# Kernel tuning notes

Hardware: AMD Instinct MI355X
Metric: run time of the kernel (lower is better)

The kernel has to match this reference:

```python
import jax, jax.numpy as jnp
import numpy as np

B, S, HID, NH = 8, 1024, 1024, 16
DH = HID // NH
ZERO = 1e-8  # undefined repo constant, assumed small epsilon


def setup_inputs() -> dict:
    key = jax.random.key(0)
    ks = jax.random.split(key, 14)
    sc = 1.0 / np.sqrt(HID)
    inp = {
        "Q": jax.random.normal(ks[0], (B, S, HID), jnp.float32),
        "K": jax.random.normal(ks[1], (B, S, HID), jnp.float32),
        "V": jax.random.normal(ks[2], (B, S, HID), jnp.float32),
        "Q_mask": jax.random.randint(ks[3], (B, S), 0, 2).astype(jnp.float32),
        "K_mask": jax.random.randint(ks[4], (B, S), 0, 2).astype(jnp.float32),
        "Wq": jax.random.normal(ks[5], (HID, HID), jnp.float32) * sc,
        "bq": jnp.zeros((HID,), jnp.float32),
        "Wk": jax.random.normal(ks[6], (HID, HID), jnp.float32) * sc,
        "bk": jnp.zeros((HID,), jnp.float32),
        "Wv": jax.random.normal(ks[7], (HID, HID), jnp.float32) * sc,
        "bv": jnp.zeros((HID,), jnp.float32),
        "Wo": jax.random.normal(ks[8], (HID, HID), jnp.float32) * sc,
        "bo": jnp.zeros((HID,), jnp.float32),
    }
    return inp


def _heads(x):  # [B,S,HID] -> [B,NH,S,DH]
    b, s, _ = x.shape
    return x.reshape(b, s, NH, DH).transpose(0, 2, 1, 3)


def reference(Q, K, V, Q_mask, K_mask, Wq, bq, Wk, bk, Wv, bv, Wo, bo):
    q = _heads(Q @ Wq.T + bq)
    k = _heads(K @ Wk.T + bk)
    v = _heads(V @ Wv.T + bv)
    # NOTE: original divides by head_size**(-0.5) == multiply by sqrt(DH)
    scores = jnp.einsum("bhqd,bhkd->bhqk", q, k) / (DH ** (-0.5))
    mask = Q_mask[:, :, None] * K_mask[:, None, :]  # [B,Sq,Sk]
    probs = jax.nn.softmax(scores, axis=-1)
    probs = jnp.where(mask[:, None, :, :] == 0, 0.0, probs)
    probs = probs / jnp.sum(probs + ZERO, axis=-1, keepdims=True)
    ctx = jnp.einsum("bhqk,bhkd->bqhd", probs, v).reshape(Q.shape[0], Q.shape[1], HID)
    return ctx @ Wo.T + bo
```

## Files before the change

kernel.cpp:

```cpp
#include <hip/hip_runtime.h>
#include <math.h>

constexpr int Bc   = 8;
constexpr int Sc   = 1024;
constexpr int HIDc = 1024;
constexpr int NHc  = 16;
constexpr int DHc  = 64;
constexpr int Mc   = Bc * Sc;
constexpr int Kc2  = 1024;
constexpr float SCALE    = 8.0f;
constexpr float EPS_TERM = 1024.0f * 1e-8f;

typedef short s16x8 __attribute__((ext_vector_type(8)));
typedef float f32x4 __attribute__((ext_vector_type(4)));

__device__ __forceinline__ ushort f2bf(float f) {
  unsigned u = __float_as_uint(f);
  u += 0x7FFFu + ((u >> 16) & 1u);
  return (ushort)(u >> 16);
}
__device__ __forceinline__ float bf2f(ushort h) {
  return __uint_as_float(((unsigned)h) << 16);
}
__device__ __forceinline__ unsigned pk2bf(float a, float b) {
  return (unsigned)f2bf(a) | ((unsigned)f2bf(b) << 16);
}

__device__ __forceinline__ void gl_lds16(const ushort* g, ushort* l) {
  __builtin_amdgcn_global_load_lds(
      (const __attribute__((address_space(1))) void*)g,
      (__attribute__((address_space(3))) void*)l, 16, 0, 0);
}

__global__ __launch_bounds__(256) void cvt_split(const float4* __restrict__ x,
    ushort4* __restrict__ hi, ushort4* __restrict__ lo, int n4)
{
  const int i = blockIdx.x * 256 + threadIdx.x;
  if (i >= n4) return;
  const float4 v = x[i];
  ushort4 h, l;
  h.x = f2bf(v.x); l.x = f2bf(v.x - bf2f(h.x));
  h.y = f2bf(v.y); l.y = f2bf(v.y - bf2f(h.y));
  h.z = f2bf(v.z); l.z = f2bf(v.z - bf2f(h.z));
  h.w = f2bf(v.w); l.w = f2bf(v.w - bf2f(h.w));
  hi[i] = h; lo[i] = l;
}

__global__ __launch_bounds__(256) void cvt_one(const float4* __restrict__ x,
    ushort4* __restrict__ hi, int n4)
{
  const int i = blockIdx.x * 256 + threadIdx.x;
  if (i >= n4) return;
  const float4 v = x[i];
  ushort4 h;
  h.x = f2bf(v.x); h.y = f2bf(v.y); h.z = f2bf(v.z); h.w = f2bf(v.w);
  hi[i] = h;
}

__global__ __launch_bounds__(256) void cvt_weights(
    const float4* __restrict__ Wq, const float4* __restrict__ Wk,
    const float4* __restrict__ Wv, const float4* __restrict__ Wo,
    ushort4* __restrict__ Wqh, ushort4* __restrict__ Wql,
    ushort4* __restrict__ Wkh, ushort4* __restrict__ Wkl,
    ushort4* __restrict__ Wvh, ushort4* __restrict__ Woh, int n4w)
{
  const int bpseg = n4w / 256;
  const int seg   = blockIdx.x / bpseg;
  const int li    = (blockIdx.x - seg * bpseg) * 256 + threadIdx.x;
  if (li >= n4w) return;
  if (seg == 0) {
    const float4 v = Wq[li];
    ushort4 h, l;
    h.x = f2bf(v.x); l.x = f2bf(v.x - bf2f(h.x));
    h.y = f2bf(v.y); l.y = f2bf(v.y - bf2f(h.y));
    h.z = f2bf(v.z); l.z = f2bf(v.z - bf2f(h.z));
    h.w = f2bf(v.w); l.w = f2bf(v.w - bf2f(h.w));
    Wqh[li] = h; Wql[li] = l;
  } else if (seg == 1) {
    const float4 v = Wk[li];
    ushort4 h, l;
    h.x = f2bf(v.x); l.x = f2bf(v.x - bf2f(h.x));
    h.y = f2bf(v.y); l.y = f2bf(v.y - bf2f(h.y));
    h.z = f2bf(v.z); l.z = f2bf(v.z - bf2f(h.z));
    h.w = f2bf(v.w); l.w = f2bf(v.w - bf2f(h.w));
    Wkh[li] = h; Wkl[li] = l;
  } else {
    const float4 v = (seg == 2) ? Wv[li] : Wo[li];
    ushort4 h;
    h.x = f2bf(v.x); h.y = f2bf(v.y); h.z = f2bf(v.z); h.w = f2bf(v.w);
    if (seg == 2) Wvh[li] = h; else Woh[li] = h;
  }
}

template<bool SPLIT3>
__global__ __launch_bounds__(256, 3) void mfma_gemm(
    const ushort* __restrict__ Ah_g, const ushort* __restrict__ Al_g,
    const ushort* __restrict__ Bh_g, const ushort* __restrict__ Bl_g,
    const float* __restrict__ bias,
    void* __restrict__ C, void* __restrict__ C2, int mode)
{
  __shared__ ushort AhL[4096];
  __shared__ ushort BhL[4096];
  __shared__ ushort AlL[SPLIT3 ? 4096 : 8];
  __shared__ ushort BlL[SPLIT3 ? 4096 : 8];

  const int t    = threadIdx.x;
  const int w    = t >> 6;
  const int ln   = t & 63;
  const int col  = ln & 15;
  const int quad = ln >> 4;
  const int wm   = w >> 1, wn = w & 1;
  const int m0   = blockIdx.y * 128;
  const int n0   = blockIdx.x * 128;

  f32x4 acc[4][4] = {};

  const int sA = w * 128;

  for (int k0 = 0; k0 < Kc2; k0 += 32) {
    __syncthreads();
#pragma unroll
    for (int j = 0; j < 2; j++) {
      const int s = sA + j * 64 + ln;
      const int r = s & 127, c = s >> 7;
      const size_t goA = (size_t)(m0 + r) * Kc2 + k0 + c * 8;
      const size_t goB = (size_t)(n0 + r) * Kc2 + k0 + c * 8;
      ushort* la = &AhL[(size_t)(sA + j * 64) * 8];
      ushort* lb = &BhL[(size_t)(sA + j * 64) * 8];
      gl_lds16(Ah_g + goA, la);
      gl_lds16(Bh_g + goB, lb);
      if constexpr (SPLIT3) {
        gl_lds16(Al_g + goA, &AlL[(size_t)(sA + j * 64) * 8]);
        gl_lds16(Bl_g + goB, &BlL[(size_t)(sA + j * 64) * 8]);
      }
    }
    __syncthreads();

    s16x8 a_h[4], b_h[4], a_l[4], b_l[4];
#pragma unroll
    for (int i = 0; i < 4; i++) {
      const int ai = (quad * 128 + wm * 64 + i * 16 + col) * 8;
      const int bi = (quad * 128 + wn * 64 + i * 16 + col) * 8;
      a_h[i] = *(const s16x8*)&AhL[ai];
      b_h[i] = *(const s16x8*)&BhL[bi];
      if constexpr (SPLIT3) {
        a_l[i] = *(const s16x8*)&AlL[ai];
        b_l[i] = *(const s16x8*)&BlL[bi];
      }
    }
#pragma unroll
    for (int i = 0; i < 4; i++)
#pragma unroll
      for (int jj = 0; jj < 4; jj++) {
        acc[i][jj] = __builtin_amdgcn_mfma_f32_16x16x32_bf16(a_h[i], b_h[jj], acc[i][jj], 0, 0, 0);
        if constexpr (SPLIT3) {
          acc[i][jj] = __builtin_amdgcn_mfma_f32_16x16x32_bf16(a_h[i], b_l[jj], acc[i][jj], 0, 0, 0);
          acc[i][jj] = __builtin_amdgcn_mfma_f32_16x16x32_bf16(a_l[i], b_h[jj], acc[i][jj], 0, 0, 0);
        }
      }
  }

  const int mb = m0 + wm * 64;
  const int nb = n0 + wn * 64;
#pragma unroll
  for (int i = 0; i < 4; i++)
#pragma unroll
    for (int jj = 0; jj < 4; jj++) {
      const int n  = nb + jj * 16 + col;
      const float bv = bias[n];
#pragma unroll
      for (int r = 0; r < 4; r++) {
        const int m   = mb + i * 16 + quad * 4 + r;
        const float v = acc[i][jj][r] + bv;
        if (mode == 0) {
          ((float*)C)[(size_t)m * HIDc + n] = v;
        } else {
          const int b_ = m >> 10, s = m & (Sc - 1);
          const int h_ = n >> 6,  d = n & (DHc - 1);
          if (mode == 1) {
            const size_t off = (((size_t)b_ * NHc + h_) * Sc + s) * DHc + d;
            const ushort hb = f2bf(v);
            ((ushort*)C)[off]  = hb;
            ((ushort*)C2)[off] = f2bf(v - bf2f(hb));
          } else {
            const size_t off = (((size_t)b_ * NHc + h_) * DHc + d) * Sc + s;
            ((ushort*)C)[off] = f2bf(v);
          }
        }
      }
    }
}

constexpr int LDP = 72;

__global__ __launch_bounds__(256, 4) void attn_mfma(
    const ushort* __restrict__ qhi, const ushort* __restrict__ qlo,
    const ushort* __restrict__ khi, const ushort* __restrict__ klo,
    const ushort* __restrict__ vt,  const float* __restrict__ Qm,
    const float* __restrict__ Km,   ushort* __restrict__ ctx)
{
  __shared__ ushort KhiL[4096];
  __shared__ ushort KloL[4096];
  __shared__ ushort VtL [4096];
  __shared__ ushort PmL [64 * LDP];
  __shared__ float  kmL[64];

  const int t    = threadIdx.x;
  const int w    = t >> 6;
  const int ln   = t & 63;
  const int col  = ln & 15;
  const int quad = ln >> 4;

  const int id  = blockIdx.x;
  const int xcd = id & 7;
  const int j   = id >> 3;
  const int bh  = xcd * 16 + (j >> 4);
  const int qt  = j & 15;
  const int b   = bh >> 4;
  const int h   = bh & 15;

  const int qbase = qt * 64 + w * 16;
  const size_t headoff = (size_t)bh * Sc * DHc;

  s16x8 qh0, qh1, ql0, ql1;
  {
    const size_t ro = headoff + (size_t)(qbase + col) * DHc + quad * 8;
    qh0 = *(const s16x8*)(qhi + ro);
    qh1 = *(const s16x8*)(qhi + ro + 32);
    ql0 = *(const s16x8*)(qlo + ro);
    ql1 = *(const s16x8*)(qlo + ro + 32);
  }

  f32x4 OT[4] = {{0,0,0,0},{0,0,0,0},{0,0,0,0},{0,0,0,0}};
  float mrow = -INFINITY;
  float Zp = 0.0f, Zmp = 0.0f;

  for (int k0 = 0; k0 < Sc; k0 += 64) {
    __syncthreads();
#pragma unroll
    for (int jj = 0; jj < 2; jj++) {
      const int c = jj * 4 + w;
      const size_t gk = headoff + (size_t)(k0 + ln) * DHc + c * 8;
      const size_t gv = headoff + (size_t)ln * Sc + k0 + c * 8;
      gl_lds16(khi + gk, &KhiL[c * 512]);
      gl_lds16(klo + gk, &KloL[c * 512]);
      gl_lds16(vt  + gv, &VtL [c * 512]);
    }
    if (t < 64) kmL[t] = Km[b * Sc + k0 + t];
    __syncthreads();

    float s[4][4];
#pragma unroll
    for (int ks = 0; ks < 4; ks++) {
      const int base0 = (quad * 64 + ks * 16 + col) * 8;
      const int base1 = ((quad + 4) * 64 + ks * 16 + col) * 8;
      const s16x8 kh0 = *(const s16x8*)&KhiL[base0];
      const s16x8 kh1 = *(const s16x8*)&KhiL[base1];
      const s16x8 kl0 = *(const s16x8*)&KloL[base0];
      const s16x8 kl1 = *(const s16x8*)&KloL[base1];
      f32x4 a = {0,0,0,0};
      a = __builtin_amdgcn_mfma_f32_16x16x32_bf16(kh0, qh0, a, 0, 0, 0);
      a = __builtin_amdgcn_mfma_f32_16x16x32_bf16(kh1, qh1, a, 0, 0, 0);
      a = __builtin_amdgcn_mfma_f32_16x16x32_bf16(kh0, ql0, a, 0, 0, 0);
      a = __builtin_amdgcn_mfma_f32_16x16x32_bf16(kh1, ql1, a, 0, 0, 0);
      a = __builtin_amdgcn_mfma_f32_16x16x32_bf16(kl0, qh0, a, 0, 0, 0);
      a = __builtin_amdgcn_mfma_f32_16x16x32_bf16(kl1, qh1, a, 0, 0, 0);
#pragma unroll
      for (int r = 0; r < 4; r++) s[ks][r] = a[r] * SCALE;
    }

    float tmax = s[0][0];
#pragma unroll
    for (int ks = 0; ks < 4; ks++)
#pragma unroll
      for (int r = 0; r < 4; r++) tmax = fmaxf(tmax, s[ks][r]);
    tmax = fmaxf(tmax, __shfl_xor(tmax, 16, 64));
    tmax = fmaxf(tmax, __shfl_xor(tmax, 32, 64));

    const float mn    = fmaxf(mrow, tmax);
    const float alpha = __expf(mrow - mn);
    mrow = mn;

    float ps = 0.0f, pms = 0.0f;
    const int prow = (w * 16 + col) * LDP;
#pragma unroll
    for (int ks = 0; ks < 4; ks++) {
      const float4 km4 = *(const float4*)&kmL[ks * 16 + quad * 4];
      const float p0 = __expf(s[ks][0] - mn), p1 = __expf(s[ks][1] - mn);
      const float p2 = __expf(s[ks][2] - mn), p3 = __expf(s[ks][3] - mn);
      const float q0 = p0 * km4.x, q1 = p1 * km4.y, q2 = p2 * km4.z, q3 = p3 * km4.w;
      ps  += (p0 + p1) + (p2 + p3);
      pms += (q0 + q1) + (q2 + q3);
      uint2 pv;
      pv.x = pk2bf(q0, q1);
      pv.y = pk2bf(q2, q3);
      *(uint2*)&PmL[prow + ks * 16 + quad * 4] = pv;
    }
    Zp  = Zp  * alpha + ps;
    Zmp = Zmp * alpha + pms;
#pragma unroll
    for (int dt = 0; dt < 4; dt++) OT[dt] *= alpha;

    const s16x8 p0 = *(const s16x8*)&PmL[prow + quad * 8];
    const s16x8 p1 = *(const s16x8*)&PmL[prow + 32 + quad * 8];
#pragma unroll
    for (int dt = 0; dt < 4; dt++) {
      const s16x8 a0 = *(const s16x8*)&VtL[(quad * 64 + dt * 16 + col) * 8];
      const s16x8 a1 = *(const s16x8*)&VtL[((quad + 4) * 64 + dt * 16 + col) * 8];
      OT[dt] = __builtin_amdgcn_mfma_f32_16x16x32_bf16(a0, p0, OT[dt], 0, 0, 0);
      OT[dt] = __builtin_amdgcn_mfma_f32_16x16x32_bf16(a1, p1, OT[dt], 0, 0, 0);
    }
  }

  Zp  += __shfl_xor(Zp,  16, 64);  Zp  += __shfl_xor(Zp,  32, 64);
  Zmp += __shfl_xor(Zmp, 16, 64);  Zmp += __shfl_xor(Zmp, 32, 64);

  const int q     = qbase + col;
  const float qmv = Qm[b * Sc + q];
  const float rden = (qmv != 0.0f) ? 1.0f / (Zmp + EPS_TERM * Zp) : 0.0f;

  ushort* crow = ctx + (size_t)(b * Sc + q) * HIDc + h * DHc + quad * 4;
#pragma unroll
  for (int dt = 0; dt < 4; dt++) {
    uint2 ov;
    ov.x = pk2bf(OT[dt][0] * rden, OT[dt][1] * rden);
    ov.y = pk2bf(OT[dt][2] * rden, OT[dt][3] * rden);
    *(uint2*)(crow + dt * 16) = ov;
  }
}

extern "C" void kernel_launch(void* const* d_in, const int* in_sizes, int n_in,
                              void* d_out, int out_size, void* d_ws, size_t ws_size,
                              hipStream_t stream)
{
  const float* Q  = (const float*)d_in[0];
  const float* K  = (const float*)d_in[1];
  const float* V  = (const float*)d_in[2];
  const float* Qm = (const float*)d_in[3];
  const float* Km = (const float*)d_in[4];
  const float* Wq = (const float*)d_in[5];
  const float* bq = (const float*)d_in[6];
  const float* Wk = (const float*)d_in[7];
  const float* bk = (const float*)d_in[8];
  const float* Wv = (const float*)d_in[9];
  const float* bv = (const float*)d_in[10];
  const float* Wo = (const float*)d_in[11];
  const float* bo = (const float*)d_in[12];
  float* out = (float*)d_out;

  const size_t NEL = (size_t)Mc * HIDc;
  const size_t WEL = (size_t)HIDc * HIDc;

  ushort* Wqh = (ushort*)d_ws;
  ushort* Wql = Wqh + WEL;
  ushort* Wkh = Wql + WEL;
  ushort* Wkl = Wkh + WEL;
  ushort* Wvh = Wkl + WEL;
  ushort* Woh = Wvh + WEL;
  ushort* qhi = Woh + WEL;
  ushort* qlo = qhi + NEL;
  ushort* khi = qlo + NEL;
  ushort* klo = khi + NEL;
  ushort* vt  = klo + NEL;
  ushort* A0  = vt  + NEL;
  ushort* A1  = A0  + NEL;

  const int n4i = (int)(NEL / 4);
  const int n4w = (int)(WEL / 4);

  cvt_weights<<<4 * (n4w / 256), 256, 0, stream>>>(
      (const float4*)Wq, (const float4*)Wk, (const float4*)Wv, (const float4*)Wo,
      (ushort4*)Wqh, (ushort4*)Wql, (ushort4*)Wkh, (ushort4*)Wkl,
      (ushort4*)Wvh, (ushort4*)Woh, n4w);

  dim3 gg(HIDc / 128, Mc / 128);

  cvt_split<<<n4i / 256, 256, 0, stream>>>((const float4*)Q, (ushort4*)A0, (ushort4*)A1, n4i);
  mfma_gemm<true><<<gg, 256, 0, stream>>>(A0, A1, Wqh, Wql, bq, qhi, qlo, 1);

  cvt_split<<<n4i / 256, 256, 0, stream>>>((const float4*)K, (ushort4*)A0, (ushort4*)A1, n4i);
  mfma_gemm<true><<<gg, 256, 0, stream>>>(A0, A1, Wkh, Wkl, bk, khi, klo, 1);

  cvt_one<<<n4i / 256, 256, 0, stream>>>((const float4*)V, (ushort4*)A0, n4i);
  mfma_gemm<false><<<gg, 256, 0, stream>>>(A0, nullptr, Wvh, nullptr, bv, vt, nullptr, 2);

  attn_mfma<<<Bc * NHc * (Sc / 64), 256, 0, stream>>>(qhi, qlo, khi, klo, vt, Qm, Km, A1);

  mfma_gemm<false><<<gg, 256, 0, stream>>>(A1, nullptr, Woh, nullptr, bo, out, nullptr, 0);
}
```

Baseline: 531.5 us.

## Fuse fp32-to-bf16 split into QKV GEMM and batch Q/K/V projections in one launch

Removes the standalone conversion kernels for Q, K and V. The GEMM now loads fp32 activations directly, splits them into hi/lo bf16 in registers and writes them to LDS. The three projections run as one launch with blockIdx.z selecting the operand. This drops the round trips of the bf16 activation copies through global memory and two kernel launches, and the larger grid fills the GPU better. The cost is that A tiles are now loaded synchronously through registers instead of via global_load_lds, the fp32 A loads are twice as wide, and the split/non-split choice becomes a runtime branch (V blocks still allocate the lo LDS buffers).

Result: no change. 524.2 us (-1.4%).

```diff
diff --git a/kernel.cpp b/kernel.cpp
--- a/kernel.cpp
+++ b/kernel.cpp
@@ -32,29 +32,17 @@
       (__attribute__((address_space(3))) void*)l, 16, 0, 0);
 }
 
-__global__ __launch_bounds__(256) void cvt_split(const float4* __restrict__ x,
-    ushort4* __restrict__ hi, ushort4* __restrict__ lo, int n4)
-{
-  const int i = blockIdx.x * 256 + threadIdx.x;
-  if (i >= n4) return;
-  const float4 v = x[i];
-  ushort4 h, l;
-  h.x = f2bf(v.x); l.x = f2bf(v.x - bf2f(h.x));
-  h.y = f2bf(v.y); l.y = f2bf(v.y - bf2f(h.y));
-  h.z = f2bf(v.z); l.z = f2bf(v.z - bf2f(h.z));
-  h.w = f2bf(v.w); l.w = f2bf(v.w - bf2f(h.w));
-  hi[i] = h; lo[i] = l;
-}
-
-__global__ __launch_bounds__(256) void cvt_one(const float4* __restrict__ x,
-    ushort4* __restrict__ hi, int n4)
-{
-  const int i = blockIdx.x * 256 + threadIdx.x;
-  if (i >= n4) return;
-  const float4 v = x[i];
-  ushort4 h;
-  h.x = f2bf(v.x); h.y = f2bf(v.y); h.z = f2bf(v.z); h.w = f2bf(v.w);
-  hi[i] = h;
+__device__ __forceinline__ void split8(const float4 v0, const float4 v1,
+                                       s16x8& hi, s16x8& lo) {
+  const float f[8] = {v0.x, v0.y, v0.z, v0.w, v1.x, v1.y, v1.z, v1.w};
+  ushort h[8], l[8];
+#pragma unroll
+  for (int i = 0; i < 8; i++) {
+    h[i] = f2bf(f[i]);
+    l[i] = f2bf(f[i] - bf2f(h[i]));
+  }
+#pragma unroll
+  for (int i = 0; i < 8; i++) { hi[i] = (short)h[i]; lo[i] = (short)l[i]; }
 }
 
 __global__ __launch_bounds__(256) void cvt_weights(
@@ -92,17 +80,29 @@
   }
 }
 
-template<bool SPLIT3>
-__global__ __launch_bounds__(256, 3) void mfma_gemm(
-    const ushort* __restrict__ Ah_g, const ushort* __restrict__ Al_g,
-    const ushort* __restrict__ Bh_g, const ushort* __restrict__ Bl_g,
-    const float* __restrict__ bias,
-    void* __restrict__ C, void* __restrict__ C2, int mode)
+__global__ __launch_bounds__(256, 3) void qkv_gemm(
+    const float* __restrict__ Qf, const float* __restrict__ Kf,
+    const float* __restrict__ Vf,
+    const ushort* __restrict__ Wqh, const ushort* __restrict__ Wql,
+    const ushort* __restrict__ Wkh, const ushort* __restrict__ Wkl,
+    const ushort* __restrict__ Wvh,
+    const float* __restrict__ bq, const float* __restrict__ bk,
+    const float* __restrict__ bv,
+    ushort* __restrict__ qhi, ushort* __restrict__ qlo,
+    ushort* __restrict__ khi, ushort* __restrict__ klo,
+    ushort* __restrict__ vt)
 {
   __shared__ ushort AhL[4096];
   __shared__ ushort BhL[4096];
-  __shared__ ushort AlL[SPLIT3 ? 4096 : 8];
-  __shared__ ushort BlL[SPLIT3 ? 4096 : 8];
+  __shared__ ushort AlL[4096];
+  __shared__ ushort BlL[4096];
+
+  const int z = blockIdx.z;
+  const bool split = (z < 2);
+  const float*  Af = (z == 0) ? Qf : (z == 1) ? Kf : Vf;
+  const ushort* Bh = (z == 0) ? Wqh : (z == 1) ? Wkh : Wvh;
+  const ushort* Bl = (z == 0) ? Wql : Wkl;
+  const float* bias = (z == 0) ? bq : (z == 1) ? bk : bv;
 
   const int t    = threadIdx.x;
   const int w    = t >> 6;
@@ -118,21 +118,33 @@
   const int sA = w * 128;
 
   for (int k0 = 0; k0 < Kc2; k0 += 32) {
-    __syncthreads();
+    float4 av[2][2];
 #pragma unroll
     for (int j = 0; j < 2; j++) {
       const int s = sA + j * 64 + ln;
       const int r = s & 127, c = s >> 7;
-      const size_t goA = (size_t)(m0 + r) * Kc2 + k0 + c * 8;
+      const float4* ga = (const float4*)(Af + (size_t)(m0 + r) * Kc2 + k0 + c * 8);
+      av[j][0] = ga[0];
+      av[j][1] = ga[1];
+    }
+
+    __syncthreads();
+
+#pragma unroll
+    for (int j = 0; j < 2; j++) {
+      const int s = sA + j * 64 + ln;
+      const int r = s & 127, c = s >> 7;
       const size_t goB = (size_t)(n0 + r) * Kc2 + k0 + c * 8;
-      ushort* la = &AhL[(size_t)(sA + j * 64) * 8];
-      ushort* lb = &BhL[(size_t)(sA + j * 64) * 8];
-      gl_lds16(Ah_g + goA, la);
-      gl_lds16(Bh_g + goB, lb);
-      if constexpr (SPLIT3) {
-        gl_lds16(Al_g + goA, &AlL[(size_t)(sA + j * 64) * 8]);
-        gl_lds16(Bl_g + goB, &BlL[(size_t)(sA + j * 64) * 8]);
-      }
+      gl_lds16(Bh + goB, &BhL[(size_t)(sA + j * 64) * 8]);
+      if (split) gl_lds16(Bl + goB, &BlL[(size_t)(sA + j * 64) * 8]);
+    }
+#pragma unroll
+    for (int j = 0; j < 2; j++) {
+      const int s = sA + j * 64 + ln;
+      s16x8 hi, lo;
+      split8(av[j][0], av[j][1], hi, lo);
+      *(s16x8*)&AhL[(size_t)s * 8] = hi;
+      if (split) *(s16x8*)&AlL[(size_t)s * 8] = lo;
     }
     __syncthreads();
 
@@ -143,7 +155,7 @@
       const int bi = (quad * 128 + wn * 64 + i * 16 + col) * 8;
       a_h[i] = *(const s16x8*)&AhL[ai];
       b_h[i] = *(const s16x8*)&BhL[bi];
-      if constexpr (SPLIT3) {
+      if (split) {
         a_l[i] = *(const s16x8*)&AlL[ai];
         b_l[i] = *(const s16x8*)&BlL[bi];
       }
@@ -153,7 +165,7 @@
 #pragma unroll
       for (int jj = 0; jj < 4; jj++) {
         acc[i][jj] = __builtin_amdgcn_mfma_f32_16x16x32_bf16(a_h[i], b_h[jj], acc[i][jj], 0, 0, 0);
-        if constexpr (SPLIT3) {
+        if (split) {
           acc[i][jj] = __builtin_amdgcn_mfma_f32_16x16x32_bf16(a_h[i], b_l[jj], acc[i][jj], 0, 0, 0);
           acc[i][jj] = __builtin_amdgcn_mfma_f32_16x16x32_bf16(a_l[i], b_h[jj], acc[i][jj], 0, 0, 0);
         }
@@ -162,31 +174,88 @@
 
   const int mb = m0 + wm * 64;
   const int nb = n0 + wn * 64;
+  ushort* Ch = (z == 0) ? qhi : khi;
+  ushort* Cl = (z == 0) ? qlo : klo;
 #pragma unroll
   for (int i = 0; i < 4; i++)
 #pragma unroll
     for (int jj = 0; jj < 4; jj++) {
       const int n  = nb + jj * 16 + col;
-      const float bv = bias[n];
+      const float bvv = bias[n];
 #pragma unroll
       for (int r = 0; r < 4; r++) {
         const int m   = mb + i * 16 + quad * 4 + r;
-        const float v = acc[i][jj][r] + bv;
-        if (mode == 0) {
-          ((float*)C)[(size_t)m * HIDc + n] = v;
+        const float v = acc[i][jj][r] + bvv;
+        const int b_ = m >> 10, s = m & (Sc - 1);
+        const int h_ = n >> 6,  d = n & (DHc - 1);
+        if (split) {
+          const size_t off = (((size_t)b_ * NHc + h_) * Sc + s) * DHc + d;
+          const ushort hb = f2bf(v);
+          Ch[off] = hb;
+          Cl[off] = f2bf(v - bf2f(hb));
         } else {
-          const int b_ = m >> 10, s = m & (Sc - 1);
-          const int h_ = n >> 6,  d = n & (DHc - 1);
-          if (mode == 1) {
-            const size_t off = (((size_t)b_ * NHc + h_) * Sc + s) * DHc + d;
-            const ushort hb = f2bf(v);
-            ((ushort*)C)[off]  = hb;
-            ((ushort*)C2)[off] = f2bf(v - bf2f(hb));
-          } else {
-            const size_t off = (((size_t)b_ * NHc + h_) * DHc + d) * Sc + s;
-            ((ushort*)C)[off] = f2bf(v);
-          }
+          const size_t off = (((size_t)b_ * NHc + h_) * DHc + d) * Sc + s;
+          vt[off] = f2bf(v);
         }
+      }
+    }
+}
+
+__global__ __launch_bounds__(256, 3) void o_gemm(
+    const ushort* __restrict__ Ag, const ushort* __restrict__ Bg,
+    const float* __restrict__ bias, float* __restrict__ C)
+{
+  __shared__ ushort AhL[4096];
+  __shared__ ushort BhL[4096];
+
+  const int t    = threadIdx.x;
+  const int w    = t >> 6;
+  const int ln   = t & 63;
+  const int col  = ln & 15;
+  const int quad = ln >> 4;
+  const int wm   = w >> 1, wn = w & 1;
+  const int m0   = blockIdx.y * 128;
+  const int n0   = blockIdx.x * 128;
+
+  f32x4 acc[4][4] = {};
+  const int sA = w * 128;
+
+  for (int k0 = 0; k0 < Kc2; k0 += 32) {
+    __syncthreads();
+#pragma unroll
+    for (int j = 0; j < 2; j++) {
+      const int s = sA + j * 64 + ln;
+      const int r = s & 127, c = s >> 7;
+      gl_lds16(Ag + (size_t)(m0 + r) * Kc2 + k0 + c * 8, &AhL[(size_t)(sA + j * 64) * 8]);
+      gl_lds16(Bg + (size_t)(n0 + r) * Kc2 + k0 + c * 8, &BhL[(size_t)(sA + j * 64) * 8]);
+    }
+    __syncthreads();
+
+    s16x8 a_h[4], b_h[4];
+#pragma unroll
+    for (int i = 0; i < 4; i++) {
+      a_h[i] = *(const s16x8*)&AhL[(quad * 128 + wm * 64 + i * 16 + col) * 8];
+      b_h[i] = *(const s16x8*)&BhL[(quad * 128 + wn * 64 + i * 16 + col) * 8];
+    }
+#pragma unroll
+    for (int i = 0; i < 4; i++)
+#pragma unroll
+      for (int jj = 0; jj < 4; jj++)
+        acc[i][jj] = __builtin_amdgcn_mfma_f32_16x16x32_bf16(a_h[i], b_h[jj], acc[i][jj], 0, 0, 0);
+  }
+
+  const int mb = m0 + wm * 64;
+  const int nb = n0 + wn * 64;
+#pragma unroll
+  for (int i = 0; i < 4; i++)
+#pragma unroll
+    for (int jj = 0; jj < 4; jj++) {
+      const int n  = nb + jj * 16 + col;
+      const float bvv = bias[n];
+#pragma unroll
+      for (int r = 0; r < 4; r++) {
+        const int m = mb + i * 16 + quad * 4 + r;
+        C[(size_t)m * HIDc + n] = acc[i][jj][r] + bvv;
       }
     }
 }
@@ -362,10 +431,8 @@
   ushort* khi = qlo + NEL;
   ushort* klo = khi + NEL;
   ushort* vt  = klo + NEL;
-  ushort* A0  = vt  + NEL;
-  ushort* A1  = A0  + NEL;
-
-  const int n4i = (int)(NEL / 4);
+  ushort* ctx = vt  + NEL;
+
   const int n4w = (int)(WEL / 4);
 
   cvt_weights<<<4 * (n4w / 256), 256, 0, stream>>>(
@@ -373,18 +440,12 @@
       (ushort4*)Wqh, (ushort4*)Wql, (ushort4*)Wkh, (ushort4*)Wkl,
       (ushort4*)Wvh, (ushort4*)Woh, n4w);
 
+  dim3 gqkv(HIDc / 128, Mc / 128, 3);
+  qkv_gemm<<<gqkv, 256, 0, stream>>>(Q, K, V,
+      Wqh, Wql, Wkh, Wkl, Wvh, bq, bk, bv, qhi, qlo, khi, klo, vt);
+
+  attn_mfma<<<Bc * NHc * (Sc / 64), 256, 0, stream>>>(qhi, qlo, khi, klo, vt, Qm, Km, ctx);
+
   dim3 gg(HIDc / 128, Mc / 128);
-
-  cvt_split<<<n4i / 256, 256, 0, stream>>>((const float4*)Q, (ushort4*)A0, (ushort4*)A1, n4i);
-  mfma_gemm<true><<<gg, 256, 0, stream>>>(A0, A1, Wqh, Wql, bq, qhi, qlo, 1);
-
-  cvt_split<<<n4i / 256, 256, 0, stream>>>((const float4*)K, (ushort4*)A0, (ushort4*)A1, n4i);
-  mfma_gemm<true><<<gg, 256, 0, stream>>>(A0, A1, Wkh, Wkl, bk, khi, klo, 1);
-
-  cvt_one<<<n4i / 256, 256, 0, stream>>>((const float4*)V, (ushort4*)A0, n4i);
-  mfma_gemm<false><<<gg, 256, 0, stream>>>(A0, nullptr, Wvh, nullptr, bv, vt, nullptr, 2);
-
-  attn_mfma<<<Bc * NHc * (Sc / 64), 256, 0, stream>>>(qhi, qlo, khi, klo, vt, Qm, Km, A1);
-
-  mfma_gemm<false><<<gg, 256, 0, stream>>>(A1, nullptr, Woh, nullptr, bo, out, nullptr, 0);
-}
+  o_gemm<<<gg, 256, 0, stream>>>(ctx, Woh, bo, out);
+}
```
